# Performance work log

Measured on AMD Instinct MI355X. Metric: run time of the kernel, lower is better.

## Reference

```python
import jax, jax.numpy as jnp
import numpy as np

MASK_SUB = 1000000.0  # the module subtracts 1e6 from masked scores (not -inf)

def setup_inputs() -> dict:
    key = jax.random.key(0)
    kq, kk, kv = jax.random.split(key, 3)
    B, S, D = 16, 2048, 64
    q = jax.random.normal(kq, (B, S, D), dtype=jnp.float32)
    k = jax.random.normal(kk, (B, S, D), dtype=jnp.float32)
    v = jax.random.normal(kv, (B, S, D), dtype=jnp.float32)
    return {"q": q, "k": k, "v": v}

def reference(q, k, v):
    d_k = k.shape[-1]
    s = k.shape[-2]
    # scores: [b, s_q, s_k]
    scores = jnp.einsum('bqd,bkd->bqk', q, k) / jnp.sqrt(jnp.asarray(d_k, q.dtype))
    # causal mask: strictly-upper-triangular entries get 1e6 subtracted (matches torch.triu diagonal=1)
    causal = jnp.triu(jnp.ones((s, s), dtype=bool), k=1)
    scores = jnp.where(causal[None, :, :], scores - MASK_SUB, scores)
    weights = jax.nn.softmax(scores, axis=-1)
    return jnp.einsum('bqk,bkd->bqd', weights, v)
```

## Files before the change

kernel.cpp:

```cpp
#include <hip/hip_runtime.h>
#include <stdint.h>


typedef __bf16 bf16x8 __attribute__((ext_vector_type(8)));
typedef float f32x4 __attribute__((ext_vector_type(4)));

#define NB 16
#define SL 2048
#define DH 64

__device__ __forceinline__ __bf16 f2bf(float f) {
    uint32_t u = __builtin_bit_cast(uint32_t, f);
    u += 0x7FFFu + ((u >> 16) & 1u);
    uint16_t h = (uint16_t)(u >> 16);
    return __builtin_bit_cast(__bf16, h);
}

__device__ __forceinline__ void load_lds16(const void* g, void* l) {
    __builtin_amdgcn_global_load_lds(
        (const __attribute__((address_space(1))) uint32_t*)g,
        (__attribute__((address_space(3))) uint32_t*)l, 16, 0, 0);
}

__global__ __launch_bounds__(256) void prepass(
        const float* __restrict__ K, const float* __restrict__ V,
        __bf16* __restrict__ Kb, __bf16* __restrict__ Vt) {
    __shared__ float tl[64][68];
    const int b    = blockIdx.x >> 5;
    const int tile = blockIdx.x & 31;
    const int s0   = tile << 6;
    const int t    = threadIdx.x;
    const int r    = t >> 2;
    const int c0   = (t & 3) * 16;

    const float* Kp = K + ((size_t)(b * SL + s0) + r) * DH + c0;
    float4 f0 = ((const float4*)Kp)[0], f1 = ((const float4*)Kp)[1];
    float4 f2 = ((const float4*)Kp)[2], f3 = ((const float4*)Kp)[3];
    bf16x8 w0, w1;
    w0[0]=f2bf(f0.x); w0[1]=f2bf(f0.y); w0[2]=f2bf(f0.z); w0[3]=f2bf(f0.w);
    w0[4]=f2bf(f1.x); w0[5]=f2bf(f1.y); w0[6]=f2bf(f1.z); w0[7]=f2bf(f1.w);
    w1[0]=f2bf(f2.x); w1[1]=f2bf(f2.y); w1[2]=f2bf(f2.z); w1[3]=f2bf(f2.w);
    w1[4]=f2bf(f3.x); w1[5]=f2bf(f3.y); w1[6]=f2bf(f3.z); w1[7]=f2bf(f3.w);
    __bf16* Kbp = Kb + ((size_t)(b * SL + s0) + r) * DH;
    const int j0 = c0 >> 3;
    *(bf16x8*)(Kbp + ((j0       ^ (r & 7)) * 8)) = w0;
    *(bf16x8*)(Kbp + (((j0 + 1) ^ (r & 7)) * 8)) = w1;

    const float* Vp = V + ((size_t)(b * SL + s0) + r) * DH + c0;
    ((float4*)&tl[r][c0])[0] = ((const float4*)Vp)[0];
    ((float4*)&tl[r][c0])[1] = ((const float4*)Vp)[1];
    ((float4*)&tl[r][c0])[2] = ((const float4*)Vp)[2];
    ((float4*)&tl[r][c0])[3] = ((const float4*)Vp)[3];
    __syncthreads();

    __bf16* img = Vt + ((size_t)(b * 32 + tile)) * 4096;
#pragma unroll
    for (int half = 0; half < 2; ++half) {
        const int c = half * 256 + t;
        const int d = c >> 3, slot = c & 7;
        const int jj = slot ^ (d & 7);
        bf16x8 w;
#pragma unroll
        for (int e = 0; e < 8; ++e) w[e] = f2bf(tl[jj * 8 + e][d]);
        *(bf16x8*)(img + c * 8) = w;
    }
}

__global__ __launch_bounds__(256, 3) void attn_fwd(
        const float* __restrict__ Q, const __bf16* __restrict__ Kb,
        const __bf16* __restrict__ Vt, float* __restrict__ part,
        float* __restrict__ lpart) {
    __shared__ __align__(16) __bf16 lK[2][4096];
    __shared__ __align__(16) __bf16 lV[2][4096];
    __shared__ __align__(16) __bf16 lP[4][2048];

    const int bid = blockIdx.x;
    const int b   = bid & 15;
    const int j   = 39 - (bid >> 4);
    int qb, c;
    if (j < 4)        { qb = j;                 c = 0; }
    else if (j < 12)  { qb = 4 + ((j - 4) >> 1);  c = (j - 4) & 1; }
    else if (j < 24)  { int k = j - 12; qb = 8 + k / 3;    c = k % 3; }
    else              { int k = j - 24; qb = 12 + (k >> 2); c = k & 3; }
    const int nt  = 2 * qb + 2;
    const int kt0 = c * 8;
    const int kt1 = min(kt0 + 8, nt);

    const int tid  = threadIdx.x;
    const int wave = tid >> 6, lane = tid & 63, quad = lane >> 4, l16 = lane & 15;
    const int xk   = l16 & 7;
    const int qg0  = qb * 128 + wave * 16 + l16;
    const int qg1  = qg0 + 64;

    const float QSC = 0.125f * 1.44269504088896340736f;
    bf16x8 qf[2][2];
#pragma unroll
    for (int st = 0; st < 2; ++st) {
        const float* qp = Q + ((size_t)b * SL + (st ? qg1 : qg0)) * DH;
#pragma unroll
        for (int s = 0; s < 2; ++s) {
            float4 a0 = ((const float4*)(qp + s * 32 + quad * 8))[0];
            float4 a1 = ((const float4*)(qp + s * 32 + quad * 8))[1];
            qf[st][s][0] = f2bf(a0.x * QSC); qf[st][s][1] = f2bf(a0.y * QSC);
            qf[st][s][2] = f2bf(a0.z * QSC); qf[st][s][3] = f2bf(a0.w * QSC);
            qf[st][s][4] = f2bf(a1.x * QSC); qf[st][s][5] = f2bf(a1.y * QSC);
            qf[st][s][6] = f2bf(a1.z * QSC); qf[st][s][7] = f2bf(a1.w * QSC);
        }
    }

    f32x4 acc0[4], acc1[4];
#pragma unroll
    for (int t = 0; t < 4; ++t) { acc0[t] = (f32x4)0.0f; acc1[t] = (f32x4)0.0f; }
    float ls0 = 0.0f, ls1 = 0.0f;

    const __bf16* Kbase = Kb + (size_t)b * SL * DH;
    const __bf16* Vbase = Vt + (size_t)b * 32 * 4096;
    __bf16* lPw = lP[wave];

    auto stage = [&](int kt2) {
        const int bufi = kt2 & 1;
        const __bf16* Ks = Kbase + (size_t)kt2 * 4096;
        const __bf16* Vs = Vbase + (size_t)kt2 * 4096;
#pragma unroll
        for (int i2 = 0; i2 < 2; ++i2) {
            load_lds16(Ks + (size_t)(i2 * 256 + tid) * 8,
                       &lK[bufi][(i2 * 256 + wave * 64) * 8]);
            load_lds16(Vs + (size_t)(i2 * 256 + tid) * 8,
                       &lV[bufi][(i2 * 256 + wave * 64) * 8]);
        }
    };

    auto softmax_store = [&](f32x4* sc, int soff, float& ls) {
#pragma unroll
        for (int t = 0; t < 4; ++t) {
            float p0 = __builtin_amdgcn_exp2f(sc[t][0]);
            float p1 = __builtin_amdgcn_exp2f(sc[t][1]);
            float p2 = __builtin_amdgcn_exp2f(sc[t][2]);
            float p3 = __builtin_amdgcn_exp2f(sc[t][3]);
            ls += (p0 + p1) + (p2 + p3);
            uint32_t u0 = __builtin_amdgcn_perm(__builtin_bit_cast(uint32_t, p1),
                                               __builtin_bit_cast(uint32_t, p0), 0x07060302u);
            uint32_t u1 = __builtin_amdgcn_perm(__builtin_bit_cast(uint32_t, p3),
                                               __builtin_bit_cast(uint32_t, p2), 0x07060302u);
            const int cw = 2 * t + (quad >> 1);
            uint2 val; val.x = u0; val.y = u1;
            *(uint2*)&lPw[soff + l16 * 64 + ((cw ^ xk) << 3) + ((quad & 1) << 2)] = val;
        }
    };

    stage(kt0);
    for (int kt = kt0; kt < kt1; ++kt) {
        __syncthreads();
        if (kt + 1 < kt1) stage(kt + 1);
        const __bf16* K_ = lK[kt & 1];
        const __bf16* V_ = lV[kt & 1];

        f32x4 sc0[4], sc1[4];
#pragma unroll
        for (int t = 0; t < 4; ++t) { sc0[t] = (f32x4)0.0f; sc1[t] = (f32x4)0.0f; }
        __builtin_amdgcn_s_setprio(1);
#pragma unroll
        for (int s = 0; s < 2; ++s) {
#pragma unroll
            for (int t = 0; t < 4; ++t) {
                bf16x8 kf = *(const bf16x8*)&K_[(t * 16 + l16) * 64 + (((s * 4 + quad) ^ xk) << 3)];
                sc0[t] = __builtin_amdgcn_mfma_f32_16x16x32_bf16(kf, qf[0][s], sc0[t], 0, 0, 0);
                sc1[t] = __builtin_amdgcn_mfma_f32_16x16x32_bf16(kf, qf[1][s], sc1[t], 0, 0, 0);
            }
        }
        __builtin_amdgcn_s_setprio(0);

        if (kt >= 2 * qb) {
            const int kb = kt * 64;
#pragma unroll
            for (int t = 0; t < 4; ++t)
#pragma unroll
                for (int r = 0; r < 4; ++r) {
                    const int key = kb + t * 16 + quad * 4 + r;
                    if (key > qg0) sc0[t][r] = -1.0e30f;
                    if (key > qg1) sc1[t][r] = -1.0e30f;
                }
        }

        softmax_store(sc0, 0,    ls0);
        softmax_store(sc1, 1024, ls1);
        asm volatile("" ::: "memory");

        bf16x8 pf00 = *(const bf16x8*)&lPw[       l16 * 64 + (((0 + quad) ^ xk) << 3)];
        bf16x8 pf01 = *(const bf16x8*)&lPw[       l16 * 64 + (((4 + quad) ^ xk) << 3)];
        bf16x8 pf10 = *(const bf16x8*)&lPw[1024 + l16 * 64 + (((0 + quad) ^ xk) << 3)];
        bf16x8 pf11 = *(const bf16x8*)&lPw[1024 + l16 * 64 + (((4 + quad) ^ xk) << 3)];

        __builtin_amdgcn_s_setprio(1);
#pragma unroll
        for (int t = 0; t < 4; ++t) {
            bf16x8 vf = *(const bf16x8*)&V_[(t * 16 + l16) * 64 + (((0 + quad) ^ xk) << 3)];
            acc0[t] = __builtin_amdgcn_mfma_f32_16x16x32_bf16(vf, pf00, acc0[t], 0, 0, 0);
            acc1[t] = __builtin_amdgcn_mfma_f32_16x16x32_bf16(vf, pf10, acc1[t], 0, 0, 0);
        }
#pragma unroll
        for (int t = 0; t < 4; ++t) {
            bf16x8 vf = *(const bf16x8*)&V_[(t * 16 + l16) * 64 + (((4 + quad) ^ xk) << 3)];
            acc0[t] = __builtin_amdgcn_mfma_f32_16x16x32_bf16(vf, pf01, acc0[t], 0, 0, 0);
            acc1[t] = __builtin_amdgcn_mfma_f32_16x16x32_bf16(vf, pf11, acc1[t], 0, 0, 0);
        }
        __builtin_amdgcn_s_setprio(0);
    }

    ls0 += __shfl_xor(ls0, 16); ls0 += __shfl_xor(ls0, 32);
    ls1 += __shfl_xor(ls1, 16); ls1 += __shfl_xor(ls1, 32);

    float* pp0 = part + ((size_t)(b * SL + qg0) * 4 + c) * DH + quad * 4;
    float* pp1 = part + ((size_t)(b * SL + qg1) * 4 + c) * DH + quad * 4;
#pragma unroll
    for (int t = 0; t < 4; ++t) {
        float4 o4;
        o4.x = acc0[t][0]; o4.y = acc0[t][1]; o4.z = acc0[t][2]; o4.w = acc0[t][3];
        *(float4*)(pp0 + t * 16) = o4;
        o4.x = acc1[t][0]; o4.y = acc1[t][1]; o4.z = acc1[t][2]; o4.w = acc1[t][3];
        *(float4*)(pp1 + t * 16) = o4;
    }
    if (quad == 0) {
        lpart[(size_t)(b * SL + qg0) * 4 + c] = ls0;
        lpart[(size_t)(b * SL + qg1) * 4 + c] = ls1;
    }
}

__global__ __launch_bounds__(256) void combine(
        const float* __restrict__ part, const float* __restrict__ lpart,
        float* __restrict__ O) {
    const int tid = threadIdx.x;
    const int r   = blockIdx.x * 16 + (tid >> 4);
    const int d4  = tid & 15;
    const int qb  = (r >> 7) & 15;
    const int nch = (2 * qb + 9) >> 3;
    float4 s = make_float4(0.f, 0.f, 0.f, 0.f);
    float ls = 0.f;
    for (int c = 0; c < nch; ++c) {
        float4 p = *(const float4*)(part + ((size_t)r * 4 + c) * DH + d4 * 4);
        s.x += p.x; s.y += p.y; s.z += p.z; s.w += p.w;
        ls += lpart[(size_t)r * 4 + c];
    }
    const float inv = 1.0f / ls;
    float4 o; o.x = s.x * inv; o.y = s.y * inv; o.z = s.z * inv; o.w = s.w * inv;
    *(float4*)(O + (size_t)r * DH + d4 * 4) = o;
}

extern "C" void kernel_launch(void* const* d_in, const int* in_sizes, int n_in,
                              void* d_out, int out_size, void* d_ws, size_t ws_size,
                              hipStream_t stream) {
    const float* q = (const float*)d_in[0];
    const float* k = (const float*)d_in[1];
    const float* v = (const float*)d_in[2];
    float* o = (float*)d_out;
    __bf16* Kb   = (__bf16*)d_ws;
    __bf16* Vt   = Kb + (size_t)NB * SL * DH;
    float*  pt   = (float*)((char*)d_ws + (8u << 20));
    float*  lp   = pt + (size_t)NB * SL * 4 * DH;
    hipLaunchKernelGGL(prepass, dim3(NB * 32), dim3(256), 0, stream, k, v, Kb, Vt);
    hipLaunchKernelGGL(attn_fwd, dim3(640), dim3(256), 0, stream, q, Kb, Vt, pt, lp);
    hipLaunchKernelGGL(combine, dim3(NB * SL / 16), dim3(256), 0, stream, pt, lp, o);
}
```

Before: 100.2 us.

## Triple-buffer K/V staging with vmcnt waits and skip fully-masked diagonal PV

The two-buffer K/V LDS ring becomes a three-buffer ring with two tiles prefetched ahead. Each iteration now waits with an explicit s_waitcnt vmcnt plus s_barrier instead of a full __syncthreads, so global-to-LDS loads overlap more compute. On the last diagonal tile, the first query subgroup is entirely masked, so its softmax store and PV MFMAs are skipped. LDS use per block rises and the launch-bounds occupancy hint drops from 3 to 2 blocks, which may reduce latency hiding from concurrent blocks.

```diff
diff --git a/kernel.cpp b/kernel.cpp
--- a/kernel.cpp
+++ b/kernel.cpp
@@ -66,12 +66,12 @@
     }
 }
 
-__global__ __launch_bounds__(256, 3) void attn_fwd(
+__global__ __launch_bounds__(256, 2) void attn_fwd(
         const float* __restrict__ Q, const __bf16* __restrict__ Kb,
         const __bf16* __restrict__ Vt, float* __restrict__ part,
         float* __restrict__ lpart) {
-    __shared__ __align__(16) __bf16 lK[2][4096];
-    __shared__ __align__(16) __bf16 lV[2][4096];
+    __shared__ __align__(16) __bf16 lK[3][4096];
+    __shared__ __align__(16) __bf16 lV[3][4096];
     __shared__ __align__(16) __bf16 lP[4][2048];
 
     const int bid = blockIdx.x;
@@ -118,7 +118,7 @@
     __bf16* lPw = lP[wave];
 
     auto stage = [&](int kt2) {
-        const int bufi = kt2 & 1;
+        const int bufi = kt2 % 3;
         const __bf16* Ks = Kbase + (size_t)kt2 * 4096;
         const __bf16* Vs = Vbase + (size_t)kt2 * 4096;
 #pragma unroll
@@ -148,12 +148,20 @@
         }
     };
 
+    __builtin_amdgcn_sched_barrier(0);
     stage(kt0);
+    __builtin_amdgcn_sched_barrier(0);
+    stage(kt0 + 1);
+
     for (int kt = kt0; kt < kt1; ++kt) {
-        __syncthreads();
-        if (kt + 1 < kt1) stage(kt + 1);
-        const __bf16* K_ = lK[kt & 1];
-        const __bf16* V_ = lV[kt & 1];
+        if (kt + 1 < kt1) asm volatile("s_waitcnt vmcnt(4)" ::: "memory");
+        else              asm volatile("s_waitcnt vmcnt(0)" ::: "memory");
+        __builtin_amdgcn_s_barrier();
+        __builtin_amdgcn_sched_barrier(0);
+        if (kt + 2 < kt1) stage(kt + 2);
+
+        const __bf16* K_ = lK[kt % 3];
+        const __bf16* V_ = lV[kt % 3];
 
         f32x4 sc0[4], sc1[4];
 #pragma unroll
@@ -182,27 +190,41 @@
                 }
         }
 
-        softmax_store(sc0, 0,    ls0);
+        const bool s0live = (kt != nt - 1);
+        if (s0live) softmax_store(sc0, 0, ls0);
         softmax_store(sc1, 1024, ls1);
         asm volatile("" ::: "memory");
 
-        bf16x8 pf00 = *(const bf16x8*)&lPw[       l16 * 64 + (((0 + quad) ^ xk) << 3)];
-        bf16x8 pf01 = *(const bf16x8*)&lPw[       l16 * 64 + (((4 + quad) ^ xk) << 3)];
         bf16x8 pf10 = *(const bf16x8*)&lPw[1024 + l16 * 64 + (((0 + quad) ^ xk) << 3)];
         bf16x8 pf11 = *(const bf16x8*)&lPw[1024 + l16 * 64 + (((4 + quad) ^ xk) << 3)];
 
         __builtin_amdgcn_s_setprio(1);
-#pragma unroll
-        for (int t = 0; t < 4; ++t) {
-            bf16x8 vf = *(const bf16x8*)&V_[(t * 16 + l16) * 64 + (((0 + quad) ^ xk) << 3)];
-            acc0[t] = __builtin_amdgcn_mfma_f32_16x16x32_bf16(vf, pf00, acc0[t], 0, 0, 0);
-            acc1[t] = __builtin_amdgcn_mfma_f32_16x16x32_bf16(vf, pf10, acc1[t], 0, 0, 0);
-        }
-#pragma unroll
-        for (int t = 0; t < 4; ++t) {
-            bf16x8 vf = *(const bf16x8*)&V_[(t * 16 + l16) * 64 + (((4 + quad) ^ xk) << 3)];
-            acc0[t] = __builtin_amdgcn_mfma_f32_16x16x32_bf16(vf, pf01, acc0[t], 0, 0, 0);
-            acc1[t] = __builtin_amdgcn_mfma_f32_16x16x32_bf16(vf, pf11, acc1[t], 0, 0, 0);
+        if (s0live) {
+            bf16x8 pf00 = *(const bf16x8*)&lPw[l16 * 64 + (((0 + quad) ^ xk) << 3)];
+            bf16x8 pf01 = *(const bf16x8*)&lPw[l16 * 64 + (((4 + quad) ^ xk) << 3)];
+#pragma unroll
+            for (int t = 0; t < 4; ++t) {
+                bf16x8 vf = *(const bf16x8*)&V_[(t * 16 + l16) * 64 + (((0 + quad) ^ xk) << 3)];
+                acc0[t] = __builtin_amdgcn_mfma_f32_16x16x32_bf16(vf, pf00, acc0[t], 0, 0, 0);
+                acc1[t] = __builtin_amdgcn_mfma_f32_16x16x32_bf16(vf, pf10, acc1[t], 0, 0, 0);
+            }
+#pragma unroll
+            for (int t = 0; t < 4; ++t) {
+                bf16x8 vf = *(const bf16x8*)&V_[(t * 16 + l16) * 64 + (((4 + quad) ^ xk) << 3)];
+                acc0[t] = __builtin_amdgcn_mfma_f32_16x16x32_bf16(vf, pf01, acc0[t], 0, 0, 0);
+                acc1[t] = __builtin_amdgcn_mfma_f32_16x16x32_bf16(vf, pf11, acc1[t], 0, 0, 0);
+            }
+        } else {
+#pragma unroll
+            for (int t = 0; t < 4; ++t) {
+                bf16x8 vf = *(const bf16x8*)&V_[(t * 16 + l16) * 64 + (((0 + quad) ^ xk) << 3)];
+                acc1[t] = __builtin_amdgcn_mfma_f32_16x16x32_bf16(vf, pf10, acc1[t], 0, 0, 0);
+            }
+#pragma unroll
+            for (int t = 0; t < 4; ++t) {
+                bf16x8 vf = *(const bf16x8*)&V_[(t * 16 + l16) * 64 + (((4 + quad) ^ xk) << 3)];
+                acc1[t] = __builtin_amdgcn_mfma_f32_16x16x32_bf16(vf, pf11, acc1[t], 0, 0, 0);
+            }
         }
         __builtin_amdgcn_s_setprio(0);
     }
```

After: 106.2 us. 1.06x slower.

## Switch attention to 32x32x16 MFMA with in-register P via permlane32 swap

Applied to the files above, without the earlier changes.

Reworks the attention kernel to use 32x32x16 bf16 MFMA tiles, with each wave owning 32 query rows instead of two 16-row strips. The softmax probabilities now stay in registers, packed with v_cvt_pk_bf16_f32 and redistributed with permlane32_swap, so the per-wave LDS P buffer and its store/load round trip are removed. Waves whose query rows lie entirely before the final diagonal key tile skip that tile. Occupancy hint rises from 3 to 4 blocks per CU; the output is now written with scalar per-element stores, which may coalesce worse.

```diff
diff --git a/kernel.cpp b/kernel.cpp
--- a/kernel.cpp
+++ b/kernel.cpp
@@ -4,6 +4,8 @@
 
 typedef __bf16 bf16x8 __attribute__((ext_vector_type(8)));
 typedef float f32x4 __attribute__((ext_vector_type(4)));
+typedef float f32x16 __attribute__((ext_vector_type(16)));
+typedef uint32_t u32x4 __attribute__((ext_vector_type(4)));
 
 #define NB 16
 #define SL 2048
@@ -14,6 +16,12 @@
     u += 0x7FFFu + ((u >> 16) & 1u);
     uint16_t h = (uint16_t)(u >> 16);
     return __builtin_bit_cast(__bf16, h);
+}
+
+__device__ __forceinline__ uint32_t cvtpk(float lo, float hi) {
+    uint32_t r;
+    asm("v_cvt_pk_bf16_f32 %0, %1, %2" : "=v"(r) : "v"(lo), "v"(hi));
+    return r;
 }
 
 __device__ __forceinline__ void load_lds16(const void* g, void* l) {
@@ -66,13 +74,12 @@
     }
 }
 
-__global__ __launch_bounds__(256, 3) void attn_fwd(
+__global__ __launch_bounds__(256, 4) void attn_fwd(
         const float* __restrict__ Q, const __bf16* __restrict__ Kb,
         const __bf16* __restrict__ Vt, float* __restrict__ part,
         float* __restrict__ lpart) {
     __shared__ __align__(16) __bf16 lK[2][4096];
     __shared__ __align__(16) __bf16 lV[2][4096];
-    __shared__ __align__(16) __bf16 lP[4][2048];
 
     const int bid = blockIdx.x;
     const int b   = bid & 15;
@@ -87,35 +94,29 @@
     const int kt1 = min(kt0 + 8, nt);
 
     const int tid  = threadIdx.x;
-    const int wave = tid >> 6, lane = tid & 63, quad = lane >> 4, l16 = lane & 15;
-    const int xk   = l16 & 7;
-    const int qg0  = qb * 128 + wave * 16 + l16;
-    const int qg1  = qg0 + 64;
+    const int wave = tid >> 6, lane = tid & 63;
+    const int h    = lane >> 5, l32 = lane & 31, x8 = lane & 7;
+    const int qg   = qb * 128 + wave * 32 + l32;
+    const int dt   = 2 * qb + (wave >> 1);
 
     const float QSC = 0.125f * 1.44269504088896340736f;
-    bf16x8 qf[2][2];
-#pragma unroll
-    for (int st = 0; st < 2; ++st) {
-        const float* qp = Q + ((size_t)b * SL + (st ? qg1 : qg0)) * DH;
-#pragma unroll
-        for (int s = 0; s < 2; ++s) {
-            float4 a0 = ((const float4*)(qp + s * 32 + quad * 8))[0];
-            float4 a1 = ((const float4*)(qp + s * 32 + quad * 8))[1];
-            qf[st][s][0] = f2bf(a0.x * QSC); qf[st][s][1] = f2bf(a0.y * QSC);
-            qf[st][s][2] = f2bf(a0.z * QSC); qf[st][s][3] = f2bf(a0.w * QSC);
-            qf[st][s][4] = f2bf(a1.x * QSC); qf[st][s][5] = f2bf(a1.y * QSC);
-            qf[st][s][6] = f2bf(a1.z * QSC); qf[st][s][7] = f2bf(a1.w * QSC);
-        }
-    }
-
-    f32x4 acc0[4], acc1[4];
-#pragma unroll
-    for (int t = 0; t < 4; ++t) { acc0[t] = (f32x4)0.0f; acc1[t] = (f32x4)0.0f; }
-    float ls0 = 0.0f, ls1 = 0.0f;
+    bf16x8 qf[4];
+    const float* qp = Q + ((size_t)b * SL + qg) * DH + h * 8;
+#pragma unroll
+    for (int s4 = 0; s4 < 4; ++s4) {
+        float4 a0 = ((const float4*)(qp + s4 * 16))[0];
+        float4 a1 = ((const float4*)(qp + s4 * 16))[1];
+        qf[s4][0] = f2bf(a0.x * QSC); qf[s4][1] = f2bf(a0.y * QSC);
+        qf[s4][2] = f2bf(a0.z * QSC); qf[s4][3] = f2bf(a0.w * QSC);
+        qf[s4][4] = f2bf(a1.x * QSC); qf[s4][5] = f2bf(a1.y * QSC);
+        qf[s4][6] = f2bf(a1.z * QSC); qf[s4][7] = f2bf(a1.w * QSC);
+    }
+
+    f32x16 acc0 = (f32x16)0.0f, acc1 = (f32x16)0.0f;
+    float ls = 0.0f;
 
     const __bf16* Kbase = Kb + (size_t)b * SL * DH;
     const __bf16* Vbase = Vt + (size_t)b * 32 * 4096;
-    __bf16* lPw = lP[wave];
 
     auto stage = [&](int kt2) {
         const int bufi = kt2 & 1;
@@ -130,24 +131,6 @@
         }
     };
 
-    auto softmax_store = [&](f32x4* sc, int soff, float& ls) {
-#pragma unroll
-        for (int t = 0; t < 4; ++t) {
-            float p0 = __builtin_amdgcn_exp2f(sc[t][0]);
-            float p1 = __builtin_amdgcn_exp2f(sc[t][1]);
-            float p2 = __builtin_amdgcn_exp2f(sc[t][2]);
-            float p3 = __builtin_amdgcn_exp2f(sc[t][3]);
-            ls += (p0 + p1) + (p2 + p3);
-            uint32_t u0 = __builtin_amdgcn_perm(__builtin_bit_cast(uint32_t, p1),
-                                               __builtin_bit_cast(uint32_t, p0), 0x07060302u);
-            uint32_t u1 = __builtin_amdgcn_perm(__builtin_bit_cast(uint32_t, p3),
-                                               __builtin_bit_cast(uint32_t, p2), 0x07060302u);
-            const int cw = 2 * t + (quad >> 1);
-            uint2 val; val.x = u0; val.y = u1;
-            *(uint2*)&lPw[soff + l16 * 64 + ((cw ^ xk) << 3) + ((quad & 1) << 2)] = val;
-        }
-    };
-
     stage(kt0);
     for (int kt = kt0; kt < kt1; ++kt) {
         __syncthreads();
@@ -155,75 +138,74 @@
         const __bf16* K_ = lK[kt & 1];
         const __bf16* V_ = lV[kt & 1];
 
-        f32x4 sc0[4], sc1[4];
-#pragma unroll
-        for (int t = 0; t < 4; ++t) { sc0[t] = (f32x4)0.0f; sc1[t] = (f32x4)0.0f; }
-        __builtin_amdgcn_s_setprio(1);
-#pragma unroll
-        for (int s = 0; s < 2; ++s) {
-#pragma unroll
-            for (int t = 0; t < 4; ++t) {
-                bf16x8 kf = *(const bf16x8*)&K_[(t * 16 + l16) * 64 + (((s * 4 + quad) ^ xk) << 3)];
-                sc0[t] = __builtin_amdgcn_mfma_f32_16x16x32_bf16(kf, qf[0][s], sc0[t], 0, 0, 0);
-                sc1[t] = __builtin_amdgcn_mfma_f32_16x16x32_bf16(kf, qf[1][s], sc1[t], 0, 0, 0);
-            }
+        const bool skip = (wave < 2) && (kt == nt - 1);
+        if (!skip) {
+            f32x16 sc0 = (f32x16)0.0f, sc1 = (f32x16)0.0f;
+            __builtin_amdgcn_s_setprio(1);
+#pragma unroll
+            for (int s4 = 0; s4 < 4; ++s4) {
+                bf16x8 kf0 = *(const bf16x8*)&K_[(l32)      * 64 + (((s4 * 2 + h) ^ x8) << 3)];
+                bf16x8 kf1 = *(const bf16x8*)&K_[(32 + l32) * 64 + (((s4 * 2 + h) ^ x8) << 3)];
+                sc0 = __builtin_amdgcn_mfma_f32_32x32x16_bf16(kf0, qf[s4], sc0, 0, 0, 0);
+                sc1 = __builtin_amdgcn_mfma_f32_32x32x16_bf16(kf1, qf[s4], sc1, 0, 0, 0);
+            }
+            __builtin_amdgcn_s_setprio(0);
+
+            if (kt >= dt) {
+                const int kb = kt * 64;
+#pragma unroll
+                for (int r = 0; r < 16; ++r) {
+                    const int krow = (r & 3) + 8 * (r >> 2) + 4 * h;
+                    if (kb + krow > qg)      sc0[r] = -1.0e30f;
+                    if (kb + 32 + krow > qg) sc1[r] = -1.0e30f;
+                }
+            }
+
+#pragma unroll
+            for (int r = 0; r < 16; ++r) {
+                sc0[r] = __builtin_amdgcn_exp2f(sc0[r]);
+                sc1[r] = __builtin_amdgcn_exp2f(sc1[r]);
+                ls += sc0[r] + sc1[r];
+            }
+
+            bf16x8 af[4];
+#pragma unroll
+            for (int ks = 0; ks < 4; ++ks) {
+                const int jj = (ks & 1) * 8;
+                const f32x16& sg = (ks & 2) ? sc1 : sc0;
+                uint32_t u0 = cvtpk(sg[jj + 0], sg[jj + 1]);
+                uint32_t u1 = cvtpk(sg[jj + 2], sg[jj + 3]);
+                uint32_t u2 = cvtpk(sg[jj + 4], sg[jj + 5]);
+                uint32_t u3 = cvtpk(sg[jj + 6], sg[jj + 7]);
+                auto r0 = __builtin_amdgcn_permlane32_swap(u0, u2, false, false);
+                auto r1 = __builtin_amdgcn_permlane32_swap(u1, u3, false, false);
+                u32x4 w; w[0] = r0[0]; w[1] = r1[0]; w[2] = r0[1]; w[3] = r1[1];
+                af[ks] = __builtin_bit_cast(bf16x8, w);
+            }
+
+            __builtin_amdgcn_s_setprio(1);
+#pragma unroll
+            for (int ks = 0; ks < 4; ++ks) {
+                bf16x8 vf0 = *(const bf16x8*)&V_[(l32)      * 64 + ((((ks << 1) + h) ^ x8) << 3)];
+                bf16x8 vf1 = *(const bf16x8*)&V_[(32 + l32) * 64 + ((((ks << 1) + h) ^ x8) << 3)];
+                acc0 = __builtin_amdgcn_mfma_f32_32x32x16_bf16(af[ks], vf0, acc0, 0, 0, 0);
+                acc1 = __builtin_amdgcn_mfma_f32_32x32x16_bf16(af[ks], vf1, acc1, 0, 0, 0);
+            }
+            __builtin_amdgcn_s_setprio(0);
         }
-        __builtin_amdgcn_s_setprio(0);
-
-        if (kt >= 2 * qb) {
-            const int kb = kt * 64;
-#pragma unroll
-            for (int t = 0; t < 4; ++t)
-#pragma unroll
-                for (int r = 0; r < 4; ++r) {
-                    const int key = kb + t * 16 + quad * 4 + r;
-                    if (key > qg0) sc0[t][r] = -1.0e30f;
-                    if (key > qg1) sc1[t][r] = -1.0e30f;
-                }
-        }
-
-        softmax_store(sc0, 0,    ls0);
-        softmax_store(sc1, 1024, ls1);
-        asm volatile("" ::: "memory");
-
-        bf16x8 pf00 = *(const bf16x8*)&lPw[       l16 * 64 + (((0 + quad) ^ xk) << 3)];
-        bf16x8 pf01 = *(const bf16x8*)&lPw[       l16 * 64 + (((4 + quad) ^ xk) << 3)];
-        bf16x8 pf10 = *(const bf16x8*)&lPw[1024 + l16 * 64 + (((0 + quad) ^ xk) << 3)];
-        bf16x8 pf11 = *(const bf16x8*)&lPw[1024 + l16 * 64 + (((4 + quad) ^ xk) << 3)];
-
-        __builtin_amdgcn_s_setprio(1);
-#pragma unroll
-        for (int t = 0; t < 4; ++t) {
-            bf16x8 vf = *(const bf16x8*)&V_[(t * 16 + l16) * 64 + (((0 + quad) ^ xk) << 3)];
-            acc0[t] = __builtin_amdgcn_mfma_f32_16x16x32_bf16(vf, pf00, acc0[t], 0, 0, 0);
-            acc1[t] = __builtin_amdgcn_mfma_f32_16x16x32_bf16(vf, pf10, acc1[t], 0, 0, 0);
-        }
-#pragma unroll
-        for (int t = 0; t < 4; ++t) {
-            bf16x8 vf = *(const bf16x8*)&V_[(t * 16 + l16) * 64 + (((4 + quad) ^ xk) << 3)];
-            acc0[t] = __builtin_amdgcn_mfma_f32_16x16x32_bf16(vf, pf01, acc0[t], 0, 0, 0);
-            acc1[t] = __builtin_amdgcn_mfma_f32_16x16x32_bf16(vf, pf11, acc1[t], 0, 0, 0);
-        }
-        __builtin_amdgcn_s_setprio(0);
-    }
-
-    ls0 += __shfl_xor(ls0, 16); ls0 += __shfl_xor(ls0, 32);
-    ls1 += __shfl_xor(ls1, 16); ls1 += __shfl_xor(ls1, 32);
-
-    float* pp0 = part + ((size_t)(b * SL + qg0) * 4 + c) * DH + quad * 4;
-    float* pp1 = part + ((size_t)(b * SL + qg1) * 4 + c) * DH + quad * 4;
-#pragma unroll
-    for (int t = 0; t < 4; ++t) {
-        float4 o4;
-        o4.x = acc0[t][0]; o4.y = acc0[t][1]; o4.z = acc0[t][2]; o4.w = acc0[t][3];
-        *(float4*)(pp0 + t * 16) = o4;
-        o4.x = acc1[t][0]; o4.y = acc1[t][1]; o4.z = acc1[t][2]; o4.w = acc1[t][3];
-        *(float4*)(pp1 + t * 16) = o4;
-    }
-    if (quad == 0) {
-        lpart[(size_t)(b * SL + qg0) * 4 + c] = ls0;
-        lpart[(size_t)(b * SL + qg1) * 4 + c] = ls1;
-    }
+    }
+
+    ls += __shfl_xor(ls, 32);
+
+#pragma unroll
+    for (int r = 0; r < 16; ++r) {
+        const int qrow = qb * 128 + wave * 32 + (r & 3) + 8 * (r >> 2) + 4 * h;
+        float* pp = part + ((size_t)(b * SL + qrow) * 4 + c) * DH + l32;
+        pp[0]  = acc0[r];
+        pp[32] = acc1[r];
+    }
+    if (h == 0)
+        lpart[(size_t)(b * SL + qg) * 4 + c] = ls;
 }
 
 __global__ __launch_bounds__(256) void combine(
```

Measured after the change: 97.11 us. -3.1%, faster.
